# Optimization experiments

Measured on AMD Instinct MI355X. Metric: run time of the kernel, lower is better.

Reference implementation:

```python
import jax, jax.numpy as jnp
import numpy as np

N = 10000
E = 640000
C = 128   # in_channels
H = 512   # hidden_dim
O = 128   # out_channels


def setup_inputs() -> dict:
    key = jax.random.key(0)
    k1, k2, k3, k4, k5, k6, k7 = jax.random.split(key, 7)
    x = jax.random.normal(k1, (N, C), dtype=jnp.float32)
    edge_index = jax.random.randint(k2, (2, E), 0, N, dtype=jnp.int64)
    # MLP params (Linear(2C, H) -> ReLU -> Linear(H, O)), torch default init scale
    w1 = jax.random.uniform(k3, (2 * C, H), jnp.float32, -1, 1) / np.sqrt(2 * C)
    b1 = jax.random.uniform(k4, (H,), jnp.float32, -1, 1) / np.sqrt(2 * C)
    w2 = jax.random.uniform(k5, (H, O), jnp.float32, -1, 1) / np.sqrt(H)
    b2 = jax.random.uniform(k6, (O,), jnp.float32, -1, 1) / np.sqrt(H)
    return {"x": x, "edge_index": edge_index, "w1": w1, "b1": b1, "w2": w2, "b2": b2}


def reference(x, edge_index, w1, b1, w2, b2):
    row, col = edge_index[0], edge_index[1]
    # scatter_mean: mean of source features x[col] into destination row
    summed = jax.ops.segment_sum(x[col], row, num_segments=N)          # [N, C]
    count = jax.ops.segment_sum(jnp.ones((E,), x.dtype), row, num_segments=N)
    neighbor_mean = summed / jnp.maximum(count, 1.0)[:, None]          # [N, C]
    h = jnp.concatenate([x, neighbor_mean], axis=1)                    # [N, 2C]
    h = jax.nn.relu(h @ w1 + b1)                                       # [N, H]
    return h @ w2 + b2                                                 # [N, O]
```

## Files before the change

kernel.cpp:

```cpp
#include <hip/hip_runtime.h>

#define C_IN 128
#define H_DIM 512
#define O_DIM 128
#define CAP   128
#define PAD   16
#define BM    32

typedef __attribute__((ext_vector_type(8))) short short8;
typedef __attribute__((ext_vector_type(4))) float f32x4;

__device__ inline unsigned short f2bf(float f) {
    unsigned int u = __float_as_uint(f);
    unsigned int r = (u + 0x7FFF + ((u >> 16) & 1)) >> 16;
    return (unsigned short)r;
}
__device__ inline float bf2f(unsigned short s) {
    return __uint_as_float(((unsigned int)s) << 16);
}

__device__ inline void tr_tile(const float* __restrict__ src, unsigned short* __restrict__ dst,
                               int R, int Ccols, int bx, int by) {
    __shared__ float tile[32][33];
    const int c0 = bx * 32, r0 = by * 32;
    const int tx = threadIdx.x & 31, ty = threadIdx.x >> 5;
#pragma unroll
    for (int i = 0; i < 32; i += 8)
        tile[ty + i][tx] = src[(long)(r0 + ty + i) * Ccols + c0 + tx];
    __syncthreads();
#pragma unroll
    for (int i = 0; i < 32; i += 8)
        dst[(long)(c0 + ty + i) * R + r0 + tx] = f2bf(tile[tx][ty + i]);
}

__global__ __launch_bounds__(256)
void prep_kernel(const float* __restrict__ w1, unsigned short* __restrict__ w1t,
                 const float* __restrict__ w2, unsigned short* __restrict__ w2t,
                 const float* __restrict__ x, unsigned short* __restrict__ h0,
                 int* __restrict__ cnt_p, int N) {
    if (blockIdx.z == 0) {
        if (blockIdx.y < (2 * C_IN) / 32) tr_tile(w1, w1t, 2 * C_IN, H_DIM, blockIdx.x, blockIdx.y);
    } else if (blockIdx.z == 1) {
        if (blockIdx.x < O_DIM / 32) tr_tile(w2, w2t, H_DIM, O_DIM, blockIdx.x, blockIdx.y);
    } else {
        const int bid = blockIdx.y * 16 + blockIdx.x;
        const int gtid = bid * 256 + threadIdx.x;
        const int nf4 = N * C_IN / 4;
        for (int i = gtid; i < nf4; i += 65536) {
            int n = i >> 5, c4 = i & 31;
            float4 v = ((const float4*)x)[i];
            ushort4 s;
            s.x = f2bf(v.x); s.y = f2bf(v.y); s.z = f2bf(v.z); s.w = f2bf(v.w);
            *(ushort4*)(h0 + (long)n * (2 * C_IN) + c4 * 4) = s;
        }
        const int n4 = N * PAD / 4;
        for (int i = gtid; i < n4; i += 65536)
            ((int4*)cnt_p)[i] = make_int4(0, 0, 0, 0);
    }
}

__global__ void fill_kernel(const int* __restrict__ ei, int* __restrict__ cnt_p,
                            unsigned short* __restrict__ bucket, int E) {
    int e = blockIdx.x * blockDim.x + threadIdx.x;
    if (e >= E) return;
    int row = ei[e];
    int col = ei[E + e];
    int slot = atomicAdd(&cnt_p[row * PAD], 1);
    if (slot < CAP) bucket[(long)row * CAP + slot] = (unsigned short)col;
}

__global__ __launch_bounds__(256)
void gather_kernel(const unsigned short* __restrict__ bucket,
                   const int* __restrict__ cnt_p, unsigned short* __restrict__ h0,
                   int N) {
    const int lane = threadIdx.x & 63;
    const int n = blockIdx.x * 4 + (threadIdx.x >> 6);
    if (n >= N) return;
    const int g = lane >> 4;
    const int l16 = lane & 15;
    const int degt = cnt_p[n * PAD];
    const int deg = min(degt, CAP);
    const long base = (long)n * CAP;

    float acc[8] = {};
    int e = 0;
    for (; e + 8 <= deg; e += 8) {
        int c0 = bucket[base + e + g];
        int c1 = bucket[base + e + 4 + g];
        short8 u0 = *(const short8*)(h0 + (long)c0 * (2 * C_IN) + l16 * 8);
        short8 u1 = *(const short8*)(h0 + (long)c1 * (2 * C_IN) + l16 * 8);
#pragma unroll
        for (int j = 0; j < 8; j++)
            acc[j] += bf2f((unsigned short)u0[j]) + bf2f((unsigned short)u1[j]);
    }
    if (e + 4 <= deg) {
        int c = bucket[base + e + g];
        short8 u = *(const short8*)(h0 + (long)c * (2 * C_IN) + l16 * 8);
#pragma unroll
        for (int j = 0; j < 8; j++) acc[j] += bf2f((unsigned short)u[j]);
        e += 4;
    }
    {
        int rem = deg - e;
        if (g < rem) {
            int c = bucket[base + e + g];
            short8 u = *(const short8*)(h0 + (long)c * (2 * C_IN) + l16 * 8);
#pragma unroll
            for (int j = 0; j < 8; j++) acc[j] += bf2f((unsigned short)u[j]);
        }
    }
#pragma unroll
    for (int j = 0; j < 8; j++) {
        acc[j] += __shfl_xor(acc[j], 16, 64);
        acc[j] += __shfl_xor(acc[j], 32, 64);
    }
    if (lane < 16) {
        float inv = 1.0f / fmaxf((float)degt, 1.0f);
        short8 mv;
#pragma unroll
        for (int j = 0; j < 8; j++) mv[j] = (short)f2bf(acc[j] * inv);
        *(short8*)(h0 + (long)n * (2 * C_IN) + C_IN + l16 * 8) = mv;
    }
}

__global__ __launch_bounds__(256)
void fused_mlp(const unsigned short* __restrict__ h0,
               const unsigned short* __restrict__ w1t,
               const float* __restrict__ bias1,
               const unsigned short* __restrict__ w2t,
               const float* __restrict__ bias2,
               float* __restrict__ out, int M) {
    __shared__ __align__(16) unsigned short h1s[BM][520];

    const int t = threadIdx.x;
    const int m0 = blockIdx.x * BM;
    const int lane = t & 63;
    const int w = t >> 6;
    const int l16 = lane & 15;
    const int q = lane >> 4;
    const int q8 = q * 8;

    short8 a_reg[2][8];
#pragma unroll
    for (int mf = 0; mf < 2; mf++) {
        int gm = m0 + mf * 16 + l16;
        if (gm < M) {
            const unsigned short* ap = h0 + (long)gm * (2 * C_IN) + q8;
#pragma unroll
            for (int s = 0; s < 8; s++) a_reg[mf][s] = *(const short8*)(ap + s * 32);
        } else {
#pragma unroll
            for (int s = 0; s < 8; s++) a_reg[mf][s] = short8{};
        }
    }

#pragma unroll
    for (int nc = 0; nc < 4; nc++) {
        const int colbase = w * 128 + nc * 32;
        f32x4 acc[2][2] = {};
#pragma unroll
        for (int s = 0; s < 8; s++) {
            short8 b0 = *(const short8*)(w1t + (long)(colbase + l16) * 256 + s * 32 + q8);
            short8 b1 = *(const short8*)(w1t + (long)(colbase + 16 + l16) * 256 + s * 32 + q8);
            acc[0][0] = __builtin_amdgcn_mfma_f32_16x16x32_bf16(a_reg[0][s], b0, acc[0][0], 0, 0, 0);
            acc[0][1] = __builtin_amdgcn_mfma_f32_16x16x32_bf16(a_reg[0][s], b1, acc[0][1], 0, 0, 0);
            acc[1][0] = __builtin_amdgcn_mfma_f32_16x16x32_bf16(a_reg[1][s], b0, acc[1][0], 0, 0, 0);
            acc[1][1] = __builtin_amdgcn_mfma_f32_16x16x32_bf16(a_reg[1][s], b1, acc[1][1], 0, 0, 0);
        }
        float bb0 = bias1[colbase + l16];
        float bb1 = bias1[colbase + 16 + l16];
#pragma unroll
        for (int mf = 0; mf < 2; mf++) {
#pragma unroll
            for (int r = 0; r < 4; r++) {
                int m = mf * 16 + q * 4 + r;
                h1s[m][colbase + l16]      = f2bf(fmaxf(acc[mf][0][r] + bb0, 0.f));
                h1s[m][colbase + 16 + l16] = f2bf(fmaxf(acc[mf][1][r] + bb1, 0.f));
            }
        }
    }
    __syncthreads();

    f32x4 acc2[2][2] = {};
    const int wn = w * 32;
#pragma unroll
    for (int ks = 0; ks < 16; ks++) {
        short8 a0 = *(const short8*)&h1s[l16][ks * 32 + q8];
        short8 a1 = *(const short8*)&h1s[16 + l16][ks * 32 + q8];
        short8 b0 = *(const short8*)(w2t + (long)(wn + l16) * H_DIM + ks * 32 + q8);
        short8 b1 = *(const short8*)(w2t + (long)(wn + 16 + l16) * H_DIM + ks * 32 + q8);
        acc2[0][0] = __builtin_amdgcn_mfma_f32_16x16x32_bf16(a0, b0, acc2[0][0], 0, 0, 0);
        acc2[0][1] = __builtin_amdgcn_mfma_f32_16x16x32_bf16(a0, b1, acc2[0][1], 0, 0, 0);
        acc2[1][0] = __builtin_amdgcn_mfma_f32_16x16x32_bf16(a1, b0, acc2[1][0], 0, 0, 0);
        acc2[1][1] = __builtin_amdgcn_mfma_f32_16x16x32_bf16(a1, b1, acc2[1][1], 0, 0, 0);
    }
#pragma unroll
    for (int mf = 0; mf < 2; mf++) {
#pragma unroll
        for (int nf = 0; nf < 2; nf++) {
            int gn = wn + nf * 16 + l16;
            float bb = bias2[gn];
#pragma unroll
            for (int r = 0; r < 4; r++) {
                int gm = m0 + mf * 16 + q * 4 + r;
                if (gm < M) out[(long)gm * O_DIM + gn] = acc2[mf][nf][r] + bb;
            }
        }
    }
}

extern "C" void kernel_launch(void* const* d_in, const int* in_sizes, int n_in,
                              void* d_out, int out_size, void* d_ws, size_t ws_size,
                              hipStream_t stream) {
    const float* x  = (const float*)d_in[0];
    const int*   ei = (const int*)d_in[1];
    const float* w1 = (const float*)d_in[2];
    const float* b1 = (const float*)d_in[3];
    const float* w2 = (const float*)d_in[4];
    const float* b2 = (const float*)d_in[5];
    float* out = (float*)d_out;

    const int N = in_sizes[0] / C_IN;
    const int E = in_sizes[1] / 2;

    unsigned short* h0b = (unsigned short*)d_ws;
    unsigned short* w1t = h0b + (size_t)N * (2 * C_IN);
    unsigned short* w2t = w1t + (size_t)H_DIM * (2 * C_IN);
    int* cnt_p = (int*)(w2t + (size_t)O_DIM * H_DIM);
    unsigned short* bucket = (unsigned short*)(cnt_p + (size_t)N * PAD);

    prep_kernel<<<dim3(16, 16, 3), 256, 0, stream>>>(w1, w1t, w2, w2t, x, h0b, cnt_p, N);
    fill_kernel<<<(E + 255) / 256, 256, 0, stream>>>(ei, cnt_p, bucket, E);
    gather_kernel<<<(N + 3) / 4, 256, 0, stream>>>(bucket, cnt_p, h0b, N);
    fused_mlp<<<(N + BM - 1) / BM, 256, 0, stream>>>(h0b, w1t, b1, w2t, b2, out, N);
}
```

Before: 144.0 us.

## Vectorize edge fill, preload bucket per wave with shuffles, deepen gather unroll

The fill kernel now handles four edges per thread using int4 loads of the edge index. The gather kernel loads each node's whole bucket row once per wave into a register and pulls neighbor ids out with shuffles instead of scattered 2-byte global loads. It also unrolls to four neighbor rows in flight per iteration. The MLP kernel gets a min-blocks-per-SM launch bound, which may constrain its register allocation. The fill grid sizing relies on E being divisible by 4.

```diff
diff --git a/kernel.cpp b/kernel.cpp
--- a/kernel.cpp
+++ b/kernel.cpp
@@ -61,12 +61,26 @@
 
 __global__ void fill_kernel(const int* __restrict__ ei, int* __restrict__ cnt_p,
                             unsigned short* __restrict__ bucket, int E) {
-    int e = blockIdx.x * blockDim.x + threadIdx.x;
-    if (e >= E) return;
-    int row = ei[e];
-    int col = ei[E + e];
-    int slot = atomicAdd(&cnt_p[row * PAD], 1);
-    if (slot < CAP) bucket[(long)row * CAP + slot] = (unsigned short)col;
+    int e = (blockIdx.x * blockDim.x + threadIdx.x) * 4;
+    if (((E & 3) == 0) && e < E) {
+        int4 r = *(const int4*)(ei + e);
+        int4 c = *(const int4*)(ei + E + e);
+        int s0 = atomicAdd(&cnt_p[r.x * PAD], 1);
+        int s1 = atomicAdd(&cnt_p[r.y * PAD], 1);
+        int s2 = atomicAdd(&cnt_p[r.z * PAD], 1);
+        int s3 = atomicAdd(&cnt_p[r.w * PAD], 1);
+        if (s0 < CAP) bucket[(long)r.x * CAP + s0] = (unsigned short)c.x;
+        if (s1 < CAP) bucket[(long)r.y * CAP + s1] = (unsigned short)c.y;
+        if (s2 < CAP) bucket[(long)r.z * CAP + s2] = (unsigned short)c.z;
+        if (s3 < CAP) bucket[(long)r.w * CAP + s3] = (unsigned short)c.w;
+    } else {
+        for (int k = e; k < E && k < e + 4; k++) {
+            int row = ei[k];
+            int col = ei[E + k];
+            int slot = atomicAdd(&cnt_p[row * PAD], 1);
+            if (slot < CAP) bucket[(long)row * CAP + slot] = (unsigned short)col;
+        }
+    }
 }
 
 __global__ __launch_bounds__(256)
@@ -80,21 +94,40 @@
     const int l16 = lane & 15;
     const int degt = cnt_p[n * PAD];
     const int deg = min(degt, CAP);
-    const long base = (long)n * CAP;
+
+    const unsigned int bb = ((const unsigned int*)bucket)[(long)n * (CAP / 2) + lane];
 
     float acc[8] = {};
     int e = 0;
-    for (; e + 8 <= deg; e += 8) {
-        int c0 = bucket[base + e + g];
-        int c1 = bucket[base + e + 4 + g];
+    for (; e + 16 <= deg; e += 16) {
+        int k0 = e + g, k1 = e + 4 + g, k2 = e + 8 + g, k3 = e + 12 + g;
+        int c0 = (__shfl(bb, k0 >> 1) >> ((k0 & 1) << 4)) & 0xffff;
+        int c1 = (__shfl(bb, k1 >> 1) >> ((k1 & 1) << 4)) & 0xffff;
+        int c2 = (__shfl(bb, k2 >> 1) >> ((k2 & 1) << 4)) & 0xffff;
+        int c3 = (__shfl(bb, k3 >> 1) >> ((k3 & 1) << 4)) & 0xffff;
         short8 u0 = *(const short8*)(h0 + (long)c0 * (2 * C_IN) + l16 * 8);
         short8 u1 = *(const short8*)(h0 + (long)c1 * (2 * C_IN) + l16 * 8);
+        short8 u2 = *(const short8*)(h0 + (long)c2 * (2 * C_IN) + l16 * 8);
+        short8 u3 = *(const short8*)(h0 + (long)c3 * (2 * C_IN) + l16 * 8);
+#pragma unroll
+        for (int j = 0; j < 8; j++)
+            acc[j] += (bf2f((unsigned short)u0[j]) + bf2f((unsigned short)u1[j]))
+                    + (bf2f((unsigned short)u2[j]) + bf2f((unsigned short)u3[j]));
+    }
+    if (e + 8 <= deg) {
+        int k0 = e + g, k1 = e + 4 + g;
+        int c0 = (__shfl(bb, k0 >> 1) >> ((k0 & 1) << 4)) & 0xffff;
+        int c1 = (__shfl(bb, k1 >> 1) >> ((k1 & 1) << 4)) & 0xffff;
+        short8 u0 = *(const short8*)(h0 + (long)c0 * (2 * C_IN) + l16 * 8);
+        short8 u1 = *(const short8*)(h0 + (long)c1 * (2 * C_IN) + l16 * 8);
 #pragma unroll
         for (int j = 0; j < 8; j++)
             acc[j] += bf2f((unsigned short)u0[j]) + bf2f((unsigned short)u1[j]);
+        e += 8;
     }
     if (e + 4 <= deg) {
-        int c = bucket[base + e + g];
+        int k = e + g;
+        int c = (__shfl(bb, k >> 1) >> ((k & 1) << 4)) & 0xffff;
         short8 u = *(const short8*)(h0 + (long)c * (2 * C_IN) + l16 * 8);
 #pragma unroll
         for (int j = 0; j < 8; j++) acc[j] += bf2f((unsigned short)u[j]);
@@ -102,8 +135,10 @@
     }
     {
         int rem = deg - e;
+        int k = e + g;
+        unsigned int bv = __shfl(bb, k >> 1);
         if (g < rem) {
-            int c = bucket[base + e + g];
+            int c = (bv >> ((k & 1) << 4)) & 0xffff;
             short8 u = *(const short8*)(h0 + (long)c * (2 * C_IN) + l16 * 8);
 #pragma unroll
             for (int j = 0; j < 8; j++) acc[j] += bf2f((unsigned short)u[j]);
@@ -123,7 +158,7 @@
     }
 }
 
-__global__ __launch_bounds__(256)
+__global__ __launch_bounds__(256, 3)
 void fused_mlp(const unsigned short* __restrict__ h0,
                const unsigned short* __restrict__ w1t,
                const float* __restrict__ bias1,
@@ -230,7 +265,7 @@
     unsigned short* bucket = (unsigned short*)(cnt_p + (size_t)N * PAD);
 
     prep_kernel<<<dim3(16, 16, 3), 256, 0, stream>>>(w1, w1t, w2, w2t, x, h0b, cnt_p, N);
-    fill_kernel<<<(E + 255) / 256, 256, 0, stream>>>(ei, cnt_p, bucket, E);
+    fill_kernel<<<(E / 4 + 255) / 256, 256, 0, stream>>>(ei, cnt_p, bucket, E);
     gather_kernel<<<(N + 3) / 4, 256, 0, stream>>>(bucket, cnt_p, h0b, N);
     fused_mlp<<<(N + BM - 1) / BM, 256, 0, stream>>>(h0b, w1t, b1, w2t, b2, out, N);
 }
```

Measured after the change: 140.9 us. 2.2% less time.
